# Kernel tuning notes

Measured on AMD Instinct MI355X. Metric: run time of the kernel, lower is better.

Reference implementation:

```python
import jax, jax.numpy as jnp
import numpy as np

NUM_ROUTING = 3  # init kwarg num_routing


def setup_inputs() -> dict:
    key = jax.random.key(0)
    k1, k2 = jax.random.split(key)
    # x: [B=128, N=1152 primary caps, C_in=8]
    x = jax.random.normal(k1, (128, 1152, 8), dtype=jnp.float32)
    # dc_w: [capsules_dim=10, num_capsules=1152, C_in=8, C_out=16]
    dc_w = jax.random.normal(k2, (10, 1152, 8, 16), dtype=jnp.float32)
    return {"x": x, "dc_w": dc_w}


def reference(x, dc_w):
    # u = x[None,:,:,None,:] @ dc_w[:,None,:,:,:]  -> [D, B, N, 1, C_out]
    u = jnp.einsum('bni,dnio->dbno', x, dc_w)[:, :, :, None, :]
    b = jnp.zeros_like(u)
    v = None
    for i in range(NUM_ROUTING):  # small fixed routing loop
        c = jax.nn.softmax(b, axis=2)                 # softmax over primary caps
        s = jnp.sum(c * u, axis=2, keepdims=True)     # [D, B, 1, 1, C_out]
        # faithful to source: norm is taken over the (singleton) axis 2,
        # so the squash coefficient is elementwise s^2 / ((1+s^2) * |s|)
        sq = s * s
        coeff = sq / ((1.0 + sq) * jnp.sqrt(sq))
        v = coeff * s
        if i != NUM_ROUTING - 1:
            b = b + jnp.sum(u * v, axis=-1, keepdims=True)  # agreement update
    return v  # [D, B, 1, 1, C_out]
```

## Files before the change

kernel.cpp:

```cpp
#include <hip/hip_runtime.h>
#include <math.h>

constexpr int NCAPS = 1152;
constexpr int CIN   = 8;
constexpr int COUT  = 16;
constexpr int BATCH = 128;
constexpr int DCAPS = 10;
constexpr int NTHREADS = 384;
constexpr int NWAVES = NTHREADS / 64;
constexpr int QPT = 12;

__global__ __launch_bounds__(NTHREADS, 4) void digitcaps_kernel(
    const float* __restrict__ x,
    const float* __restrict__ w,
    float* __restrict__ out)
{
    __shared__ float4 red[NWAVES][4];
    __shared__ float  sbuf[NWAVES];
    __shared__ float4 vsh[4];

    const int i   = blockIdx.x;
    const int xcd = i & 7;
    const int k   = i >> 3;
    const int d   = (xcd >> 2) * 5 + (k % 5);
    const int b   = (k / 5) * 4 + (xcd & 3);

    const int t    = threadIdx.x;
    const int wave = t >> 6;
    const int lane = t & 63;
    const int nsub = lane >> 2;
    const int oq   = lane & 3;

    const float* xb = x + (size_t)b * NCAPS * CIN;
    const float* wd = w + (size_t)d * NCAPS * CIN * COUT;

    float4 u4[QPT];
    #pragma unroll
    for (int j = 0; j < QPT; ++j) {
        const int n = j * 96 + wave * 16 + nsub;
        const float* xr = xb + (size_t)n * CIN;
        const float* wr = wd + (size_t)n * CIN * COUT + oq * 4;
        float4 xa = ((const float4*)xr)[0];
        float4 xc = ((const float4*)xr)[1];
        float xi[CIN] = {xa.x, xa.y, xa.z, xa.w, xc.x, xc.y, xc.z, xc.w};
        float4 acc = {0.f, 0.f, 0.f, 0.f};
        #pragma unroll
        for (int ii = 0; ii < CIN; ++ii) {
            float4 wv = *(const float4*)(wr + ii * COUT);
            acc.x = fmaf(xi[ii], wv.x, acc.x);
            acc.y = fmaf(xi[ii], wv.y, acc.y);
            acc.z = fmaf(xi[ii], wv.z, acc.z);
            acc.w = fmaf(xi[ii], wv.w, acc.w);
        }
        u4[j] = acc;
    }

    float bb[QPT];
    #pragma unroll
    for (int j = 0; j < QPT; ++j) bb[j] = 0.f;

    #pragma unroll
    for (int it = 0; it < 3; ++it) {
        float cc[QPT];
        float scale;
        if (it == 0) {
            #pragma unroll
            for (int j = 0; j < QPT; ++j) cc[j] = 1.f;
            scale = 1.f / (float)NCAPS;
        } else {
            float m = bb[0];
            #pragma unroll
            for (int j = 1; j < QPT; ++j) m = fmaxf(m, bb[j]);
            #pragma unroll
            for (int off = 1; off < 64; off <<= 1)
                m = fmaxf(m, __shfl_xor(m, off));
            if (lane == 0) sbuf[wave] = m;
            __syncthreads();
            float M = sbuf[0];
            #pragma unroll
            for (int wv = 1; wv < NWAVES; ++wv) M = fmaxf(M, sbuf[wv]);
            __syncthreads();
            float z = 0.f;
            #pragma unroll
            for (int j = 0; j < QPT; ++j) {
                cc[j] = __expf(bb[j] - M);
                z += cc[j];
            }
            #pragma unroll
            for (int off = 1; off < 64; off <<= 1)
                z += __shfl_xor(z, off);
            if (lane == 0) sbuf[wave] = z;
            __syncthreads();
            float Z = 0.f;
            #pragma unroll
            for (int wv = 0; wv < NWAVES; ++wv) Z += sbuf[wv];
            scale = 4.f / Z;
            __syncthreads();
        }

        float4 p = {0.f, 0.f, 0.f, 0.f};
        #pragma unroll
        for (int j = 0; j < QPT; ++j) {
            p.x = fmaf(cc[j], u4[j].x, p.x);
            p.y = fmaf(cc[j], u4[j].y, p.y);
            p.z = fmaf(cc[j], u4[j].z, p.z);
            p.w = fmaf(cc[j], u4[j].w, p.w);
        }
        #pragma unroll
        for (int off = 4; off < 64; off <<= 1) {
            p.x += __shfl_xor(p.x, off);
            p.y += __shfl_xor(p.y, off);
            p.z += __shfl_xor(p.z, off);
            p.w += __shfl_xor(p.w, off);
        }
        if (nsub == 0) red[wave][oq] = p;
        __syncthreads();

        if (t < 4) {
            float4 s = red[0][t];
            #pragma unroll
            for (int wv = 1; wv < NWAVES; ++wv) {
                float4 r = red[wv][t];
                s.x += r.x; s.y += r.y; s.z += r.z; s.w += r.w;
            }
            s.x *= scale; s.y *= scale; s.z *= scale; s.w *= scale;
            float4 v;
            v.x = s.x * fabsf(s.x) / (1.f + s.x * s.x);
            v.y = s.y * fabsf(s.y) / (1.f + s.y * s.y);
            v.z = s.z * fabsf(s.z) / (1.f + s.z * s.z);
            v.w = s.w * fabsf(s.w) / (1.f + s.w * s.w);
            vsh[t] = v;
            if (it == 2)
                ((float4*)(out + ((size_t)d * BATCH + b) * COUT))[t] = v;
        }
        __syncthreads();

        if (it < 2) {
            float4 v = vsh[oq];
            #pragma unroll
            for (int j = 0; j < QPT; ++j) {
                float dotv = u4[j].x * v.x + u4[j].y * v.y +
                             u4[j].z * v.z + u4[j].w * v.w;
                dotv += __shfl_xor(dotv, 1);
                dotv += __shfl_xor(dotv, 2);
                bb[j] += dotv;
            }
        }
        __syncthreads();
    }
}

extern "C" void kernel_launch(void* const* d_in, const int* in_sizes, int n_in,
                              void* d_out, int out_size, void* d_ws, size_t ws_size,
                              hipStream_t stream) {
    const float* x = (const float*)d_in[0];
    const float* w = (const float*)d_in[1];
    float* out = (float*)d_out;
    digitcaps_kernel<<<DCAPS * BATCH, NTHREADS, 0, stream>>>(x, w, out);
}
```

Baseline: 105.6 us.

## Double block size and merge softmax denominator reduction with weighted sum

Raises the block size to 768 threads, so each thread holds 6 capsule rows instead of 12, and updates launch bounds to match. Computes the softmax denominator in the same pass and shuffle tree as the weighted sum of u, which drops one block-wide reduction and two barriers per routing iteration. It also removes the trailing barrier and unrolls the u computation explicitly. The intent is fewer synchronisations and better latency hiding per block, at the cost of more waves per barrier and possible changes in occupancy.

```diff
diff --git a/kernel.cpp b/kernel.cpp
--- a/kernel.cpp
+++ b/kernel.cpp
@@ -6,11 +6,11 @@
 constexpr int COUT  = 16;
 constexpr int BATCH = 128;
 constexpr int DCAPS = 10;
-constexpr int NTHREADS = 384;
+constexpr int NTHREADS = 768;
 constexpr int NWAVES = NTHREADS / 64;
-constexpr int QPT = 12;
+constexpr int QPT = NCAPS * 4 / NTHREADS;
 
-__global__ __launch_bounds__(NTHREADS, 4) void digitcaps_kernel(
+__global__ __launch_bounds__(NTHREADS, 6) void digitcaps_kernel(
     const float* __restrict__ x,
     const float* __restrict__ w,
     float* __restrict__ out)
@@ -32,26 +32,41 @@
     const int oq   = lane & 3;
 
     const float* xb = x + (size_t)b * NCAPS * CIN;
-    const float* wd = w + (size_t)d * NCAPS * CIN * COUT;
+    const float* wd = w + (size_t)d * NCAPS * CIN * COUT + oq * 4;
 
     float4 u4[QPT];
     #pragma unroll
     for (int j = 0; j < QPT; ++j) {
-        const int n = j * 96 + wave * 16 + nsub;
-        const float* xr = xb + (size_t)n * CIN;
-        const float* wr = wd + (size_t)n * CIN * COUT + oq * 4;
-        float4 xa = ((const float4*)xr)[0];
-        float4 xc = ((const float4*)xr)[1];
-        float xi[CIN] = {xa.x, xa.y, xa.z, xa.w, xc.x, xc.y, xc.z, xc.w};
-        float4 acc = {0.f, 0.f, 0.f, 0.f};
-        #pragma unroll
-        for (int ii = 0; ii < CIN; ++ii) {
-            float4 wv = *(const float4*)(wr + ii * COUT);
-            acc.x = fmaf(xi[ii], wv.x, acc.x);
-            acc.y = fmaf(xi[ii], wv.y, acc.y);
-            acc.z = fmaf(xi[ii], wv.z, acc.z);
-            acc.w = fmaf(xi[ii], wv.w, acc.w);
-        }
+        const int n = j * 192 + wave * 16 + nsub;
+        const float4* xr = (const float4*)(xb + (size_t)n * CIN);
+        float4 xa = xr[0];
+        float4 xc = xr[1];
+        const float* wr = wd + (size_t)n * CIN * COUT;
+        float4 w0 = *(const float4*)(wr + 0 * COUT);
+        float4 w1 = *(const float4*)(wr + 1 * COUT);
+        float4 w2 = *(const float4*)(wr + 2 * COUT);
+        float4 w3 = *(const float4*)(wr + 3 * COUT);
+        float4 w4 = *(const float4*)(wr + 4 * COUT);
+        float4 w5 = *(const float4*)(wr + 5 * COUT);
+        float4 w6 = *(const float4*)(wr + 6 * COUT);
+        float4 w7 = *(const float4*)(wr + 7 * COUT);
+        float4 acc;
+        acc.x = xa.x * w0.x; acc.y = xa.x * w0.y;
+        acc.z = xa.x * w0.z; acc.w = xa.x * w0.w;
+        acc.x = fmaf(xa.y, w1.x, acc.x); acc.y = fmaf(xa.y, w1.y, acc.y);
+        acc.z = fmaf(xa.y, w1.z, acc.z); acc.w = fmaf(xa.y, w1.w, acc.w);
+        acc.x = fmaf(xa.z, w2.x, acc.x); acc.y = fmaf(xa.z, w2.y, acc.y);
+        acc.z = fmaf(xa.z, w2.z, acc.z); acc.w = fmaf(xa.z, w2.w, acc.w);
+        acc.x = fmaf(xa.w, w3.x, acc.x); acc.y = fmaf(xa.w, w3.y, acc.y);
+        acc.z = fmaf(xa.w, w3.z, acc.z); acc.w = fmaf(xa.w, w3.w, acc.w);
+        acc.x = fmaf(xc.x, w4.x, acc.x); acc.y = fmaf(xc.x, w4.y, acc.y);
+        acc.z = fmaf(xc.x, w4.z, acc.z); acc.w = fmaf(xc.x, w4.w, acc.w);
+        acc.x = fmaf(xc.y, w5.x, acc.x); acc.y = fmaf(xc.y, w5.y, acc.y);
+        acc.z = fmaf(xc.y, w5.z, acc.z); acc.w = fmaf(xc.y, w5.w, acc.w);
+        acc.x = fmaf(xc.z, w6.x, acc.x); acc.y = fmaf(xc.z, w6.y, acc.y);
+        acc.z = fmaf(xc.z, w6.z, acc.z); acc.w = fmaf(xc.z, w6.w, acc.w);
+        acc.x = fmaf(xc.w, w7.x, acc.x); acc.y = fmaf(xc.w, w7.y, acc.y);
+        acc.z = fmaf(xc.w, w7.z, acc.z); acc.w = fmaf(xc.w, w7.w, acc.w);
         u4[j] = acc;
     }
 
@@ -61,12 +76,14 @@
 
     #pragma unroll
     for (int it = 0; it < 3; ++it) {
-        float cc[QPT];
-        float scale;
+        float4 p = {0.f, 0.f, 0.f, 0.f};
+        float z = 0.f;
         if (it == 0) {
             #pragma unroll
-            for (int j = 0; j < QPT; ++j) cc[j] = 1.f;
-            scale = 1.f / (float)NCAPS;
+            for (int j = 0; j < QPT; ++j) {
+                p.x += u4[j].x; p.y += u4[j].y;
+                p.z += u4[j].z; p.w += u4[j].w;
+            }
         } else {
             float m = bb[0];
             #pragma unroll
@@ -80,31 +97,17 @@
             #pragma unroll
             for (int wv = 1; wv < NWAVES; ++wv) M = fmaxf(M, sbuf[wv]);
             __syncthreads();
-            float z = 0.f;
             #pragma unroll
             for (int j = 0; j < QPT; ++j) {
-                cc[j] = __expf(bb[j] - M);
-                z += cc[j];
+                float e = __expf(bb[j] - M);
+                z += e;
+                p.x = fmaf(e, u4[j].x, p.x);
+                p.y = fmaf(e, u4[j].y, p.y);
+                p.z = fmaf(e, u4[j].z, p.z);
+                p.w = fmaf(e, u4[j].w, p.w);
             }
-            #pragma unroll
-            for (int off = 1; off < 64; off <<= 1)
-                z += __shfl_xor(z, off);
-            if (lane == 0) sbuf[wave] = z;
-            __syncthreads();
-            float Z = 0.f;
-            #pragma unroll
-            for (int wv = 0; wv < NWAVES; ++wv) Z += sbuf[wv];
-            scale = 4.f / Z;
-            __syncthreads();
-        }
-
-        float4 p = {0.f, 0.f, 0.f, 0.f};
-        #pragma unroll
-        for (int j = 0; j < QPT; ++j) {
-            p.x = fmaf(cc[j], u4[j].x, p.x);
-            p.y = fmaf(cc[j], u4[j].y, p.y);
-            p.z = fmaf(cc[j], u4[j].z, p.z);
-            p.w = fmaf(cc[j], u4[j].w, p.w);
+            z += __shfl_xor(z, 1);
+            z += __shfl_xor(z, 2);
         }
         #pragma unroll
         for (int off = 4; off < 64; off <<= 1) {
@@ -112,8 +115,10 @@
             p.y += __shfl_xor(p.y, off);
             p.z += __shfl_xor(p.z, off);
             p.w += __shfl_xor(p.w, off);
+            if (it != 0) z += __shfl_xor(z, off);
         }
         if (nsub == 0) red[wave][oq] = p;
+        if (it != 0 && lane == 0) sbuf[wave] = z;
         __syncthreads();
 
         if (t < 4) {
@@ -122,6 +127,15 @@
             for (int wv = 1; wv < NWAVES; ++wv) {
                 float4 r = red[wv][t];
                 s.x += r.x; s.y += r.y; s.z += r.z; s.w += r.w;
+            }
+            float scale;
+            if (it == 0) {
+                scale = 1.f / (float)NCAPS;
+            } else {
+                float Z = sbuf[0];
+                #pragma unroll
+                for (int wv = 1; wv < NWAVES; ++wv) Z += sbuf[wv];
+                scale = 4.f / Z;
             }
             s.x *= scale; s.y *= scale; s.z *= scale; s.w *= scale;
             float4 v;
@@ -146,7 +160,6 @@
                 bb[j] += dotv;
             }
         }
-        __syncthreads();
     }
 }
 
```

New measurement: 107.9 us. +2.2%, slower.

## Process two batch rows per block to reuse weight loads, fuse softmax passes

Applied to the files above, without the earlier changes.

Each block now handles two batch elements for one digit capsule, so each W float4 loaded from global memory is reused for two prediction vectors. The block size doubles to 768 threads with half the grid, and the block-to-(d,b) mapping is changed. The softmax sum is fused into the weighted-sum pass, which removes one reduction barrier round and the trailing sync. The risks are lower occupancy (launch bounds of 1) and higher register pressure from holding both u sets.

```diff
diff --git a/kernel.cpp b/kernel.cpp
--- a/kernel.cpp
+++ b/kernel.cpp
@@ -6,24 +6,27 @@
 constexpr int COUT  = 16;
 constexpr int BATCH = 128;
 constexpr int DCAPS = 10;
-constexpr int NTHREADS = 384;
+constexpr int NTHREADS = 768;
 constexpr int NWAVES = NTHREADS / 64;
-constexpr int QPT = 12;
+constexpr int JPT = 6;
 
-__global__ __launch_bounds__(NTHREADS, 4) void digitcaps_kernel(
+__global__ __launch_bounds__(NTHREADS, 1) void digitcaps_kernel(
     const float* __restrict__ x,
     const float* __restrict__ w,
     float* __restrict__ out)
 {
-    __shared__ float4 red[NWAVES][4];
-    __shared__ float  sbuf[NWAVES];
-    __shared__ float4 vsh[4];
+    __shared__ float4 red[2][NWAVES][4];
+    __shared__ float  sbuf[2][NWAVES];
+    __shared__ float  zbuf[2][NWAVES];
+    __shared__ float4 vsh[2][4];
 
     const int i   = blockIdx.x;
     const int xcd = i & 7;
     const int k   = i >> 3;
-    const int d   = (xcd >> 2) * 5 + (k % 5);
-    const int b   = (k / 5) * 4 + (xcd & 3);
+    const int d   = k >> 3;
+    const int bp  = xcd * 8 + (k & 7);
+    const int b0  = 2 * bp;
+    const int b1  = b0 + 1;
 
     const int t    = threadIdx.x;
     const int wave = t >> 6;
@@ -31,97 +34,119 @@
     const int nsub = lane >> 2;
     const int oq   = lane & 3;
 
-    const float* xb = x + (size_t)b * NCAPS * CIN;
-    const float* wd = w + (size_t)d * NCAPS * CIN * COUT;
+    const float* xb0 = x + (size_t)b0 * NCAPS * CIN;
+    const float* xb1 = x + (size_t)b1 * NCAPS * CIN;
+    const float* wd  = w + (size_t)d * NCAPS * CIN * COUT + oq * 4;
 
-    float4 u4[QPT];
+    float4 u0[JPT], u1[JPT];
     #pragma unroll
-    for (int j = 0; j < QPT; ++j) {
-        const int n = j * 96 + wave * 16 + nsub;
-        const float* xr = xb + (size_t)n * CIN;
-        const float* wr = wd + (size_t)n * CIN * COUT + oq * 4;
-        float4 xa = ((const float4*)xr)[0];
-        float4 xc = ((const float4*)xr)[1];
-        float xi[CIN] = {xa.x, xa.y, xa.z, xa.w, xc.x, xc.y, xc.z, xc.w};
-        float4 acc = {0.f, 0.f, 0.f, 0.f};
+    for (int j = 0; j < JPT; ++j) {
+        const int n = j * 192 + wave * 16 + nsub;
+        const float* wr = wd + (size_t)n * CIN * COUT;
+        float4 W[CIN];
+        #pragma unroll
+        for (int ii = 0; ii < CIN; ++ii)
+            W[ii] = *(const float4*)(wr + ii * COUT);
+        const float4* xr0 = (const float4*)(xb0 + (size_t)n * CIN);
+        const float4* xr1 = (const float4*)(xb1 + (size_t)n * CIN);
+        float4 xa0 = xr0[0], xc0 = xr0[1];
+        float4 xa1 = xr1[0], xc1 = xr1[1];
+        float xs0[CIN] = {xa0.x, xa0.y, xa0.z, xa0.w, xc0.x, xc0.y, xc0.z, xc0.w};
+        float xs1[CIN] = {xa1.x, xa1.y, xa1.z, xa1.w, xc1.x, xc1.y, xc1.z, xc1.w};
+        float4 a0 = {0.f, 0.f, 0.f, 0.f};
+        float4 a1 = {0.f, 0.f, 0.f, 0.f};
         #pragma unroll
         for (int ii = 0; ii < CIN; ++ii) {
-            float4 wv = *(const float4*)(wr + ii * COUT);
-            acc.x = fmaf(xi[ii], wv.x, acc.x);
-            acc.y = fmaf(xi[ii], wv.y, acc.y);
-            acc.z = fmaf(xi[ii], wv.z, acc.z);
-            acc.w = fmaf(xi[ii], wv.w, acc.w);
+            a0.x = fmaf(xs0[ii], W[ii].x, a0.x);
+            a0.y = fmaf(xs0[ii], W[ii].y, a0.y);
+            a0.z = fmaf(xs0[ii], W[ii].z, a0.z);
+            a0.w = fmaf(xs0[ii], W[ii].w, a0.w);
+            a1.x = fmaf(xs1[ii], W[ii].x, a1.x);
+            a1.y = fmaf(xs1[ii], W[ii].y, a1.y);
+            a1.z = fmaf(xs1[ii], W[ii].z, a1.z);
+            a1.w = fmaf(xs1[ii], W[ii].w, a1.w);
         }
-        u4[j] = acc;
+        u0[j] = a0;
+        u1[j] = a1;
     }
 
-    float bb[QPT];
+    float bb0[JPT], bb1[JPT];
     #pragma unroll
-    for (int j = 0; j < QPT; ++j) bb[j] = 0.f;
+    for (int j = 0; j < JPT; ++j) { bb0[j] = 0.f; bb1[j] = 0.f; }
 
     #pragma unroll
     for (int it = 0; it < 3; ++it) {
-        float cc[QPT];
-        float scale;
+        float4 p0 = {0.f, 0.f, 0.f, 0.f};
+        float4 p1 = {0.f, 0.f, 0.f, 0.f};
+        float z0 = 0.f, z1 = 0.f;
         if (it == 0) {
             #pragma unroll
-            for (int j = 0; j < QPT; ++j) cc[j] = 1.f;
-            scale = 1.f / (float)NCAPS;
+            for (int j = 0; j < JPT; ++j) {
+                p0.x += u0[j].x; p0.y += u0[j].y; p0.z += u0[j].z; p0.w += u0[j].w;
+                p1.x += u1[j].x; p1.y += u1[j].y; p1.z += u1[j].z; p1.w += u1[j].w;
+            }
         } else {
-            float m = bb[0];
+            float m0 = bb0[0], m1 = bb1[0];
             #pragma unroll
-            for (int j = 1; j < QPT; ++j) m = fmaxf(m, bb[j]);
-            #pragma unroll
-            for (int off = 1; off < 64; off <<= 1)
-                m = fmaxf(m, __shfl_xor(m, off));
-            if (lane == 0) sbuf[wave] = m;
-            __syncthreads();
-            float M = sbuf[0];
-            #pragma unroll
-            for (int wv = 1; wv < NWAVES; ++wv) M = fmaxf(M, sbuf[wv]);
-            __syncthreads();
-            float z = 0.f;
-            #pragma unroll
-            for (int j = 0; j < QPT; ++j) {
-                cc[j] = __expf(bb[j] - M);
-                z += cc[j];
+            for (int j = 1; j < JPT; ++j) {
+                m0 = fmaxf(m0, bb0[j]);
+                m1 = fmaxf(m1, bb1[j]);
             }
             #pragma unroll
-            for (int off = 1; off < 64; off <<= 1)
-                z += __shfl_xor(z, off);
-            if (lane == 0) sbuf[wave] = z;
+            for (int off = 1; off < 64; off <<= 1) {
+                m0 = fmaxf(m0, __shfl_xor(m0, off));
+                m1 = fmaxf(m1, __shfl_xor(m1, off));
+            }
+            if (lane == 0) { sbuf[0][wave] = m0; sbuf[1][wave] = m1; }
             __syncthreads();
-            float Z = 0.f;
+            float M0 = sbuf[0][0], M1 = sbuf[1][0];
             #pragma unroll
-            for (int wv = 0; wv < NWAVES; ++wv) Z += sbuf[wv];
-            scale = 4.f / Z;
-            __syncthreads();
-        }
-
-        float4 p = {0.f, 0.f, 0.f, 0.f};
-        #pragma unroll
-        for (int j = 0; j < QPT; ++j) {
-            p.x = fmaf(cc[j], u4[j].x, p.x);
-            p.y = fmaf(cc[j], u4[j].y, p.y);
-            p.z = fmaf(cc[j], u4[j].z, p.z);
-            p.w = fmaf(cc[j], u4[j].w, p.w);
+            for (int wv = 1; wv < NWAVES; ++wv) {
+                M0 = fmaxf(M0, sbuf[0][wv]);
+                M1 = fmaxf(M1, sbuf[1][wv]);
+            }
+            #pragma unroll
+            for (int j = 0; j < JPT; ++j) {
+                float e0 = __expf(bb0[j] - M0);
+                float e1 = __expf(bb1[j] - M1);
+                z0 += e0; z1 += e1;
+                p0.x = fmaf(e0, u0[j].x, p0.x); p0.y = fmaf(e0, u0[j].y, p0.y);
+                p0.z = fmaf(e0, u0[j].z, p0.z); p0.w = fmaf(e0, u0[j].w, p0.w);
+                p1.x = fmaf(e1, u1[j].x, p1.x); p1.y = fmaf(e1, u1[j].y, p1.y);
+                p1.z = fmaf(e1, u1[j].z, p1.z); p1.w = fmaf(e1, u1[j].w, p1.w);
+            }
+            z0 += __shfl_xor(z0, 1); z0 += __shfl_xor(z0, 2);
+            z1 += __shfl_xor(z1, 1); z1 += __shfl_xor(z1, 2);
         }
         #pragma unroll
         for (int off = 4; off < 64; off <<= 1) {
-            p.x += __shfl_xor(p.x, off);
-            p.y += __shfl_xor(p.y, off);
-            p.z += __shfl_xor(p.z, off);
-            p.w += __shfl_xor(p.w, off);
+            p0.x += __shfl_xor(p0.x, off); p0.y += __shfl_xor(p0.y, off);
+            p0.z += __shfl_xor(p0.z, off); p0.w += __shfl_xor(p0.w, off);
+            p1.x += __shfl_xor(p1.x, off); p1.y += __shfl_xor(p1.y, off);
+            p1.z += __shfl_xor(p1.z, off); p1.w += __shfl_xor(p1.w, off);
+            if (it != 0) { z0 += __shfl_xor(z0, off); z1 += __shfl_xor(z1, off); }
         }
-        if (nsub == 0) red[wave][oq] = p;
+        if (nsub == 0) { red[0][wave][oq] = p0; red[1][wave][oq] = p1; }
+        if (it != 0 && lane == 0) { zbuf[0][wave] = z0; zbuf[1][wave] = z1; }
         __syncthreads();
 
-        if (t < 4) {
-            float4 s = red[0][t];
+        if (t < 8) {
+            const int bsel = t >> 2;
+            const int o    = t & 3;
+            float4 s = red[bsel][0][o];
             #pragma unroll
             for (int wv = 1; wv < NWAVES; ++wv) {
-                float4 r = red[wv][t];
+                float4 r = red[bsel][wv][o];
                 s.x += r.x; s.y += r.y; s.z += r.z; s.w += r.w;
+            }
+            float scale;
+            if (it == 0) {
+                scale = 1.f / (float)NCAPS;
+            } else {
+                float Z = zbuf[bsel][0];
+                #pragma unroll
+                for (int wv = 1; wv < NWAVES; ++wv) Z += zbuf[bsel][wv];
+                scale = 4.f / Z;
             }
             s.x *= scale; s.y *= scale; s.z *= scale; s.w *= scale;
             float4 v;
@@ -129,24 +154,29 @@
             v.y = s.y * fabsf(s.y) / (1.f + s.y * s.y);
             v.z = s.z * fabsf(s.z) / (1.f + s.z * s.z);
             v.w = s.w * fabsf(s.w) / (1.f + s.w * s.w);
-            vsh[t] = v;
-            if (it == 2)
-                ((float4*)(out + ((size_t)d * BATCH + b) * COUT))[t] = v;
+            vsh[bsel][o] = v;
+            if (it == 2) {
+                const int b = bsel ? b1 : b0;
+                ((float4*)(out + ((size_t)d * BATCH + b) * COUT))[o] = v;
+            }
         }
         __syncthreads();
 
         if (it < 2) {
-            float4 v = vsh[oq];
+            float4 v0 = vsh[0][oq];
+            float4 v1 = vsh[1][oq];
             #pragma unroll
-            for (int j = 0; j < QPT; ++j) {
-                float dotv = u4[j].x * v.x + u4[j].y * v.y +
-                             u4[j].z * v.z + u4[j].w * v.w;
-                dotv += __shfl_xor(dotv, 1);
-                dotv += __shfl_xor(dotv, 2);
-                bb[j] += dotv;
+            for (int j = 0; j < JPT; ++j) {
+                float dv0 = u0[j].x * v0.x + u0[j].y * v0.y +
+                            u0[j].z * v0.z + u0[j].w * v0.w;
+                float dv1 = u1[j].x * v1.x + u1[j].y * v1.y +
+                            u1[j].z * v1.z + u1[j].w * v1.w;
+                dv0 += __shfl_xor(dv0, 1); dv0 += __shfl_xor(dv0, 2);
+                dv1 += __shfl_xor(dv1, 1); dv1 += __shfl_xor(dv1, 2);
+                bb0[j] += dv0;
+                bb1[j] += dv1;
             }
         }
-        __syncthreads();
     }
 }
 
@@ -156,5 +186,5 @@
     const float* x = (const float*)d_in[0];
     const float* w = (const float*)d_in[1];
     float* out = (float*)d_out;
-    digitcaps_kernel<<<DCAPS * BATCH, NTHREADS, 0, stream>>>(x, w, out);
+    digitcaps_kernel<<<DCAPS * BATCH / 2, NTHREADS, 0, stream>>>(x, w, out);
 }
```

New measurement: 108.0 us. +2.3%, slower.
